# Optimization experiments

Hardware: AMD Instinct MI355X
Metric: run time of the kernel (lower is better)

Reference implementation:

```python
import jax, jax.numpy as jnp
import numpy as np

B, S, HID = 2, 2048, 2048
H, HKV, D = 16, 4, 128
BS = 64            # block_size
TAU = 0.5          # threshold_tau
NB = S // BS       # number of blocks
SCALE = 1.0 / (D ** 0.5)


def _rotate_half(x):
    x1, x2 = x[..., : D // 2], x[..., D // 2 :]
    return jnp.concatenate([-x2, x1], axis=-1)


def setup_inputs() -> dict:
    key = jax.random.key(0)
    k0, k1, k2, k3, k4 = jax.random.split(key, 5)
    hidden_states = jax.random.normal(k0, (B, S, HID), jnp.float32)
    # standard rotary embeddings, [B, S, D] (ndim==3 path of _apply_rotary_pos_emb)
    pos = jnp.arange(S, dtype=jnp.float32)
    inv_freq = 1.0 / (10000.0 ** (jnp.arange(0, D, 2, dtype=jnp.float32) / D))
    emb = jnp.concatenate([pos[:, None] * inv_freq[None, :]] * 2, axis=-1)  # [S, D]
    cos = jnp.broadcast_to(jnp.cos(emb)[None], (B, S, D)).astype(jnp.float32)
    sin = jnp.broadcast_to(jnp.sin(emb)[None], (B, S, D)).astype(jnp.float32)
    Wq = jax.random.normal(k1, (HID, H * D), jnp.float32) * 0.02
    Wk = jax.random.normal(k2, (HID, HKV * D), jnp.float32) * 0.02
    Wv = jax.random.normal(k3, (HID, HKV * D), jnp.float32) * 0.02
    Wo = jax.random.normal(k4, (HID, HID), jnp.float32) * 0.02
    return {"hidden_states": hidden_states, "cos": cos, "sin": sin,
            "Wq": Wq, "Wk": Wk, "Wv": Wv, "Wo": Wo}


def reference(hidden_states, cos, sin, Wq, Wk, Wv, Wo):
    # QKV projections -> [B, heads, S, D]
    q = (hidden_states @ Wq).reshape(B, S, H, D).transpose(0, 2, 1, 3)
    k = (hidden_states @ Wk).reshape(B, S, HKV, D).transpose(0, 2, 1, 3)
    v = (hidden_states @ Wv).reshape(B, S, HKV, D).transpose(0, 2, 1, 3)
    # RoPE (cos/sin [B,S,D] -> broadcast over heads)
    c, s = cos[:, None], sin[:, None]
    q = q * c + _rotate_half(q) * s
    k = k * c + _rotate_half(k) * s
    # GQA repeat_interleave on head dim
    n_rep = H // HKV
    k = jnp.repeat(k, n_rep, axis=1)
    v = jnp.repeat(v, n_rep, axis=1)
    # ---- AttnGate: block-mean pooled Q/K scores -> hard block mask ----
    q_blk = q.reshape(B, H, NB, BS, D).mean(axis=3)  # [B,H,NB,D]
    k_blk = k.reshape(B, H, NB, BS, D).mean(axis=3)
    gate_logits = jnp.einsum('bhid,bhjd->bhij', q_blk, k_blk) * SCALE
    hard = jax.nn.sigmoid(gate_logits) >= TAU                      # [B,H,NB,NB]
    hard = hard | jnp.eye(NB, dtype=bool)                          # keep diagonal blocks
    hard = hard & jnp.tril(jnp.ones((NB, NB), dtype=bool))         # block-causal
    # expand block mask to token level and intersect with causal mask
    tok_mask = jnp.repeat(jnp.repeat(hard, BS, axis=2), BS, axis=3)  # [B,H,S,S]
    tok_mask = tok_mask & jnp.tril(jnp.ones((S, S), dtype=bool))
    # ---- block-sparse (masked) attention ----
    scores = jnp.einsum('bhsd,bhtd->bhst', q, k) * SCALE
    scores = jnp.where(tok_mask, scores, jnp.float32(-1e30))
    probs = jax.nn.softmax(scores.astype(jnp.float32), axis=-1).astype(v.dtype)
    out = jnp.einsum('bhst,bhtd->bhsd', probs, v)
    out = out.transpose(0, 2, 1, 3).reshape(B, S, HID)
    return out @ Wo
```

## Files before the change

kernel.cpp:

```cpp
#include <hip/hip_runtime.h>
#include <stdint.h>

typedef unsigned short u16;
typedef _Float16 half8 __attribute__((ext_vector_type(8)));
typedef float floatx4 __attribute__((ext_vector_type(4)));
typedef u16 u16x4 __attribute__((ext_vector_type(4)));

#define B_ 2
#define S_ 2048
#define HID_ 2048
#define H_ 16
#define HKV_ 4
#define D_ 128
#define NB_ 32
#define SCALE_ 0.08838834764831845f
#define SC_L2 0.12753102331884178f
#define SMAX_L2 5.770780163555852f

__device__ __forceinline__ u16 f2h_bits(float f) {
  _Float16 h = (_Float16)f;
  return __builtin_bit_cast(u16, h);
}

__device__ __forceinline__ void transpose_body(const float* __restrict__ src, u16* __restrict__ dst,
                                               int Kdim, int N, int ldd, int nsplit,
                                               int k0, int n0, float (*tile)[65]) {
#pragma unroll
  for (int p = 0; p < 16; ++p) {
    int e = threadIdx.x + p * 256;
    int r = e >> 6, c = e & 63;
    tile[r][c] = src[(size_t)(k0 + r) * N + n0 + c];
  }
  __syncthreads();
#pragma unroll
  for (int p = 0; p < 16; ++p) {
    int e = threadIdx.x + p * 256;
    int k = e & 63, n = e >> 6;
    float v = tile[k][n];
    for (int s = 0; s < nsplit; ++s) {
      _Float16 hh = (_Float16)v;
      dst[(size_t)(n0 + n) * ldd + s * Kdim + k0 + k] = __builtin_bit_cast(u16, hh);
      v -= (float)hh;
    }
  }
}

__global__ __launch_bounds__(256) void k_prep(const float* __restrict__ hs, u16* __restrict__ A2,
                                              const float* __restrict__ Wq, const float* __restrict__ Wk,
                                              const float* __restrict__ Wv,
                                              u16* __restrict__ B2T, u16* __restrict__ WvT) {
  __shared__ float tile[64][65];
  int id = blockIdx.x;
  if (id < 8192) {
    int idx = id * 256 + threadIdx.x;
    int f0 = idx * 4;
    float4 v = *reinterpret_cast<const float4*>(hs + f0);
    float vv[4] = {v.x, v.y, v.z, v.w};
    u16x4 h0, h1;
#pragma unroll
    for (int e = 0; e < 4; ++e) {
      _Float16 a = (_Float16)vv[e];
      float r = vv[e] - (float)a;
      _Float16 b = (_Float16)r;
      h0[e] = __builtin_bit_cast(u16, a);
      h1[e] = __builtin_bit_cast(u16, b);
    }
    int row = f0 >> 11;
    int col = f0 & 2047;
    *reinterpret_cast<u16x4*>(A2 + (size_t)row * 4096 + col) = h0;
    *reinterpret_cast<u16x4*>(A2 + (size_t)row * 4096 + 2048 + col) = h1;
  } else if (id < 9216) {
    int t = id - 8192;
    transpose_body(Wq, B2T, 2048, 2048, 4096, 2, (t & 31) * 64, (t >> 5) * 64, tile);
  } else if (id < 9472) {
    int t = id - 9216;
    transpose_body(Wk, B2T + (size_t)2048 * 4096, 2048, 512, 4096, 2, (t & 31) * 64, (t >> 5) * 64, tile);
  } else {
    int t = id - 9472;
    transpose_body(Wv, WvT, 2048, 512, 2048, 1, (t & 31) * 64, (t >> 5) * 64, tile);
  }
}

__global__ __launch_bounds__(256) void k_transpose_split(const float* __restrict__ src, u16* __restrict__ dst,
                                                         int Kdim, int N, int ldd, int nsplit) {
  __shared__ float tile[64][65];
  transpose_body(src, dst, Kdim, N, ldd, nsplit, blockIdx.x * 64, blockIdx.y * 64, tile);
}


#define FENCE() __builtin_amdgcn_sched_barrier(0)
#define BAR() do { FENCE(); __builtin_amdgcn_s_barrier(); FENCE(); } while (0)
#define WAITVM(N) do { FENCE(); asm volatile("s_waitcnt vmcnt(" #N ")" ::: "memory"); FENCE(); } while (0)

__device__ __forceinline__ int kmap(int map, int t) {
  return ((map >> ((t >> 5) * 4)) & 15) * 2048 + (t & 31) * 64;
}

__device__ __forceinline__ void stage_half(const u16* __restrict__ src, int sr0, int lda, int kb,
                                           u16* dst, int w, int lane) {
#pragma unroll
  for (int rr = 0; rr < 2; ++rr) {
    int chunk = rr * 8 + w;
    int row = chunk * 8 + (lane >> 3);
    int slot = (lane & 7) ^ (lane >> 3);
    const u16* gp = src + (size_t)(sr0 + row) * lda + kb + slot * 8;
    __builtin_amdgcn_global_load_lds((const __attribute__((address_space(1))) unsigned int*)gp,
                                     (__attribute__((address_space(3))) unsigned int*)(dst + chunk * 512),
                                     16, 0, 0);
  }
}

#define RD_A(mh) do { \
  _Pragma("unroll") \
  for (int m_ = 0; m_ < 4; ++m_) { \
    aF[m_][0] = *reinterpret_cast<const half8*>(&sm[(mh)*8192 + (wm*64 + m_*16 + l15)*64 + ((quad ^ l7) * 8)]); \
    aF[m_][1] = *reinterpret_cast<const half8*>(&sm[(mh)*8192 + (wm*64 + m_*16 + l15)*64 + (((4 + quad) ^ l7) * 8)]); \
  } } while (0)

#define RD_B(nh, BF) do { \
  _Pragma("unroll") \
  for (int n_ = 0; n_ < 2; ++n_) { \
    BF[n_][0] = *reinterpret_cast<const half8*>(&sm[16384 + (nh)*8192 + (wn*32 + n_*16 + l15)*64 + ((quad ^ l7) * 8)]); \
    BF[n_][1] = *reinterpret_cast<const half8*>(&sm[16384 + (nh)*8192 + (wn*32 + n_*16 + l15)*64 + (((4 + quad) ^ l7) * 8)]); \
  } } while (0)

#define MM(mh, nh, BF) do { \
  __builtin_amdgcn_s_setprio(1); \
  _Pragma("unroll") \
  for (int m_ = 0; m_ < 4; ++m_) \
  _Pragma("unroll") \
  for (int n_ = 0; n_ < 2; ++n_) { \
    acc[(mh)*4 + m_][(nh)*2 + n_] = __builtin_amdgcn_mfma_f32_16x16x32_f16(aF[m_][0], BF[n_][0], acc[(mh)*4 + m_][(nh)*2 + n_], 0, 0, 0); \
    acc[(mh)*4 + m_][(nh)*2 + n_] = __builtin_amdgcn_mfma_f32_16x16x32_f16(aF[m_][1], BF[n_][1], acc[(mh)*4 + m_][(nh)*2 + n_], 0, 0, 0); \
  } \
  __builtin_amdgcn_s_setprio(0); } while (0)

__device__ __forceinline__ void gemm256(const u16* __restrict__ A, const u16* __restrict__ BT,
                                        float* __restrict__ C, u16* __restrict__ Ch, u16* sm,
                                        int row0, int col0, int NT,
                                        int lda, int ldb, int ldc, int ldch,
                                        int amap, int bmap) {
  const int tid = (int)threadIdx.x;
  const int lane = tid & 63;
  const int w = tid >> 6;
  const int wm = w >> 2, wn = w & 3;
  const int quad = lane >> 4, l15 = lane & 15, l7 = lane & 7;

  floatx4 acc[8][4];
#pragma unroll
  for (int i = 0; i < 8; ++i)
#pragma unroll
    for (int j = 0; j < 4; ++j) acc[i][j] = (floatx4){0.f, 0.f, 0.f, 0.f};

  half8 aF[4][2], bF0[2][2], bF1[2][2];

  {
    int ka = kmap(amap, 0), kb = kmap(bmap, 0);
    stage_half(A,  row0,       lda, ka, sm + 0,     w, lane);
    stage_half(BT, col0,       ldb, kb, sm + 16384, w, lane);
    stage_half(BT, col0 + 128, ldb, kb, sm + 24576, w, lane);
    stage_half(A,  row0 + 128, lda, ka, sm + 8192,  w, lane);
  }
  WAITVM(4);
  BAR();

  for (int t = 0; t < NT; ++t) {
    int tn = t + 1; if (tn >= NT) tn = 0;
    int kan = kmap(amap, tn), kbn = kmap(bmap, tn);

    RD_A(0); RD_B(0, bF0);
    WAITVM(2);
    BAR(); MM(0, 0, bF0); BAR();
    RD_B(1, bF1);
    stage_half(A,  row0, lda, kan, sm + 0,     w, lane);
    stage_half(BT, col0, ldb, kbn, sm + 16384, w, lane);
    WAITVM(4);
    BAR(); MM(0, 1, bF1); BAR();
    RD_A(1);
    stage_half(BT, col0 + 128, ldb, kbn, sm + 24576, w, lane);
    BAR(); MM(1, 1, bF1); BAR();
    stage_half(A, row0 + 128, lda, kan, sm + 8192, w, lane);
    WAITVM(4);
    BAR(); MM(1, 0, bF0); BAR();
  }
  WAITVM(0);

#pragma unroll
  for (int i = 0; i < 8; ++i) {
    int mh = i >> 2, m = i & 3;
#pragma unroll
    for (int j = 0; j < 4; ++j) {
      int nh = j >> 1, n = j & 1;
#pragma unroll
      for (int r = 0; r < 4; ++r) {
        int rr = row0 + mh * 128 + wm * 64 + m * 16 + quad * 4 + r;
        int cc = col0 + nh * 128 + wn * 32 + n * 16 + l15;
        if (Ch)
          Ch[(size_t)rr * ldch + cc] = f2h_bits(acc[i][j][r]);
        else
          C[(size_t)rr * ldc + cc] = acc[i][j][r];
      }
    }
  }
}


__device__ __forceinline__ void stage_halfA64(const u16* __restrict__ src, int sr0, int lda, int kb,
                                              u16* dst, int w, int lane) {
  int row = w * 8 + (lane >> 3);
  int slot = (lane & 7) ^ (lane >> 3);
  const u16* gp = src + (size_t)(sr0 + row) * lda + kb + slot * 8;
  __builtin_amdgcn_global_load_lds((const __attribute__((address_space(1))) unsigned int*)gp,
                                   (__attribute__((address_space(3))) unsigned int*)(dst + w * 512),
                                   16, 0, 0);
}

#define RD_A128(mh) do { \
  _Pragma("unroll") \
  for (int m_ = 0; m_ < 2; ++m_) { \
    aF[m_][0] = *reinterpret_cast<const half8*>(&sm[(mh)*4096 + (wm*32 + m_*16 + l15)*64 + ((quad ^ l7) * 8)]); \
    aF[m_][1] = *reinterpret_cast<const half8*>(&sm[(mh)*4096 + (wm*32 + m_*16 + l15)*64 + (((4 + quad) ^ l7) * 8)]); \
  } } while (0)

#define RD_B128(nh, BF) do { \
  _Pragma("unroll") \
  for (int n_ = 0; n_ < 2; ++n_) { \
    BF[n_][0] = *reinterpret_cast<const half8*>(&sm[8192 + (nh)*8192 + (wn*32 + n_*16 + l15)*64 + ((quad ^ l7) * 8)]); \
    BF[n_][1] = *reinterpret_cast<const half8*>(&sm[8192 + (nh)*8192 + (wn*32 + n_*16 + l15)*64 + (((4 + quad) ^ l7) * 8)]); \
  } } while (0)

#define MM128(mh, nh, BF) do { \
  __builtin_amdgcn_s_setprio(1); \
  _Pragma("unroll") \
  for (int m_ = 0; m_ < 2; ++m_) \
  _Pragma("unroll") \
  for (int n_ = 0; n_ < 2; ++n_) { \
    acc[(mh)*2 + m_][(nh)*2 + n_] = __builtin_amdgcn_mfma_f32_16x16x32_f16(aF[m_][0], BF[n_][0], acc[(mh)*2 + m_][(nh)*2 + n_], 0, 0, 0); \
    acc[(mh)*2 + m_][(nh)*2 + n_] = __builtin_amdgcn_mfma_f32_16x16x32_f16(aF[m_][1], BF[n_][1], acc[(mh)*2 + m_][(nh)*2 + n_], 0, 0, 0); \
  } \
  __builtin_amdgcn_s_setprio(0); } while (0)

__device__ __forceinline__ void gemm128(const u16* __restrict__ A, const u16* __restrict__ BT,
                                        float* __restrict__ C, u16* sm,
                                        int row0, int col0, int NT,
                                        int lda, int ldb, int ldc) {
  const int tid = (int)threadIdx.x;
  const int lane = tid & 63;
  const int w = tid >> 6;
  const int wm = w >> 2, wn = w & 3;
  const int quad = lane >> 4, l15 = lane & 15, l7 = lane & 7;

  floatx4 acc[4][4];
#pragma unroll
  for (int i = 0; i < 4; ++i)
#pragma unroll
    for (int j = 0; j < 4; ++j) acc[i][j] = (floatx4){0.f, 0.f, 0.f, 0.f};

  half8 aF[2][2], bF0[2][2], bF1[2][2];

  stage_halfA64(A,  row0,      lda, 0, sm + 0,     w, lane);
  stage_half  (BT, col0,       ldb, 0, sm + 8192,  w, lane);
  stage_half  (BT, col0 + 128, ldb, 0, sm + 16384, w, lane);
  stage_halfA64(A,  row0 + 64, lda, 0, sm + 4096,  w, lane);
  WAITVM(3);
  BAR();

  for (int t = 0; t < NT; ++t) {
    int tn = t + 1; if (tn >= NT) tn = 0;
    int kn = tn * 64;

    RD_A128(0); RD_B128(0, bF0);
    WAITVM(1);
    BAR(); MM128(0, 0, bF0); BAR();
    RD_B128(1, bF1);
    stage_halfA64(A,  row0, lda, kn, sm + 0,    w, lane);
    stage_half  (BT, col0, ldb, kn, sm + 8192,  w, lane);
    WAITVM(3);
    BAR(); MM128(0, 1, bF1); BAR();
    RD_A128(1);
    stage_half(BT, col0 + 128, ldb, kn, sm + 16384, w, lane);
    BAR(); MM128(1, 1, bF1); BAR();
    stage_halfA64(A, row0 + 64, lda, kn, sm + 4096, w, lane);
    WAITVM(3);
    BAR(); MM128(1, 0, bF0); BAR();
  }
  WAITVM(0);

#pragma unroll
  for (int i = 0; i < 4; ++i) {
    int mh = i >> 1, m = i & 1;
#pragma unroll
    for (int j = 0; j < 4; ++j) {
      int nh = j >> 1, n = j & 1;
#pragma unroll
      for (int r = 0; r < 4; ++r) {
        int rr = row0 + mh * 64 + wm * 32 + m * 16 + quad * 4 + r;
        int cc = col0 + nh * 128 + wn * 32 + n * 16 + l15;
        C[(size_t)rr * ldc + cc] = acc[i][j][r];
      }
    }
  }
}

__global__ __launch_bounds__(512) void k_gemm_qkv(const u16* __restrict__ A2, const u16* __restrict__ B2T,
                                                  const u16* __restrict__ WvT, float* __restrict__ qkv,
                                                  u16* __restrict__ corr) {
  __shared__ u16 sm[32768];
  int id = blockIdx.x;
  if (id < 160) {
    int lg = (id & 7) * 20 + (id >> 3);
    int row0 = (lg / 10) * 256, col0 = (lg % 10) * 256;
    gemm256(A2, B2T, nullptr, corr, sm, row0, col0, 64, 4096, 4096, 0, 2560, 0x01, 0x10);
  } else if (id < 320) {
    int t = id - 160;
    int lg = (t & 7) * 20 + (t >> 3);
    int row0 = (lg / 10) * 256, col0 = (lg % 10) * 256;
    gemm256(A2, B2T, qkv, nullptr, sm, row0, col0, 32, 4096, 4096, 3072, 0, 0, 0);
  } else {
    int t = id - 320;
    int row0 = (t >> 1) * 256, col0 = (t & 1) * 256;
    gemm256(A2, WvT, qkv + 2560, nullptr, sm, row0, col0, 32, 4096, 2048, 3072, 0, 0, 0);
  }
}

__global__ __launch_bounds__(512) void k_gemm_wo(const u16* __restrict__ attn, const u16* __restrict__ WoT,
                                                 float* __restrict__ out) {
  __shared__ u16 sm[24576];
  int id = blockIdx.x;
  gemm128(attn, WoT, out, sm, (id >> 3) * 128, (id & 7) * 256, 32, 2048, 2048, 2048);
}

__global__ __launch_bounds__(256) void k_rope_mean(const float* __restrict__ qkv, const u16* __restrict__ corr,
                                                   const float* __restrict__ cosb, const float* __restrict__ sinb,
                                                   u16* __restrict__ qbf, u16* __restrict__ kbf,
                                                   float* __restrict__ qblk, float* __restrict__ kblk) {
  int cc = blockIdx.x, i = blockIdx.y, b = blockIdx.z;
  int c = cc * 256 + threadIdx.x;
  bool isq = c < 2048;
  int hh = isq ? (c >> 7) : ((c - 2048) >> 7);
  int d = isq ? (c & 127) : ((c - 2048) & 127);
  int pairc = (d < 64) ? c + 64 : c - 64;
  float sgn = (d < 64) ? -1.0f : 1.0f;
  int row0 = b * S_ + i * 64;
  float sum = 0.0f;
  for (int s = 0; s < 64; ++s) {
    int row = row0 + s;
    float x1 = qkv[(size_t)row * 3072 + c]
             + (float)__builtin_bit_cast(_Float16, corr[(size_t)row * 2560 + c]);
    float x2 = qkv[(size_t)row * 3072 + pairc]
             + (float)__builtin_bit_cast(_Float16, corr[(size_t)row * 2560 + pairc]);
    float cv = cosb[(size_t)row * 128 + d];
    float sv = sinb[(size_t)row * 128 + d];
    float val = x1 * cv + sgn * x2 * sv;
    sum += val;
    if (isq)
      qbf[((size_t)(b * H_ + hh) * S_ + i * 64 + s) * 128 + d] = f2h_bits(val);
    else
      kbf[((size_t)(b * HKV_ + hh) * S_ + i * 64 + s) * 128 + d] = f2h_bits(val);
  }
  if (isq)
    qblk[((size_t)(b * H_ + hh) * NB_ + i) * 128 + d] = sum * 0.015625f;
  else
    kblk[((size_t)(b * HKV_ + hh) * NB_ + i) * 128 + d] = sum * 0.015625f;
}

__global__ __launch_bounds__(256) void k_vlayout(const float* __restrict__ qkv, u16* __restrict__ vT) {
  int i = blockIdx.x, hk = blockIdx.y, b = blockIdx.z;
  __shared__ u16 tile[64 * 130];
#pragma unroll
  for (int p = 0; p < 32; ++p) {
    int e = threadIdx.x + p * 256;
    int s = e >> 7, d = e & 127;
    float v = qkv[(size_t)(b * S_ + i * 64 + s) * 3072 + 2560 + hk * 128 + d];
    tile[s * 130 + d] = f2h_bits(v);
  }
  __syncthreads();
#pragma unroll
  for (int p = 0; p < 32; ++p) {
    int e = threadIdx.x + p * 256;
    int d2 = e >> 6, s2 = e & 63;
    vT[((size_t)(b * HKV_ + hk) * 128 + d2) * S_ + i * 64 + s2] = tile[s2 * 130 + d2];
  }
}

__global__ __launch_bounds__(256) void k_gate(const float* __restrict__ qblk, const float* __restrict__ kblk,
                                              int* __restrict__ mask) {
  int h = blockIdx.x, b = blockIdx.y;
  int hk = h >> 2;
  __shared__ float qs[32 * 128];
  __shared__ float ks[32 * 128];
  size_t qb0 = (size_t)(b * H_ + h) * NB_ * 128;
  size_t kb0 = (size_t)(b * HKV_ + hk) * NB_ * 128;
#pragma unroll
  for (int p = 0; p < 16; ++p) {
    int e = threadIdx.x + p * 256;
    qs[e] = qblk[qb0 + e];
    ks[e] = kblk[kb0 + e];
  }
  __syncthreads();
#pragma unroll
  for (int p = 0; p < 4; ++p) {
    int l = threadIdx.x + p * 256;
    int i = l >> 5, j = l & 31;
    int m;
    if (j > i) m = 0;
    else if (j == i) m = 1;
    else {
      float dot = 0.0f;
      for (int d = 0; d < 128; ++d) dot += qs[i * 128 + d] * ks[j * 128 + d];
      m = (dot >= 0.0f) ? 1 : 0;
    }
    mask[((size_t)(b * H_ + h) * NB_ + i) * NB_ + j] = m;
  }
}

__global__ __launch_bounds__(256) void k_flash(const u16* __restrict__ qbf, const u16* __restrict__ kbf,
                                               const u16* __restrict__ vT, const int* __restrict__ mask,
                                               u16* __restrict__ attn) {
  const int id = blockIdx.x;
  const int i = 31 - (id >> 5);
  const int hb = id & 31;
  const int h = hb & 15, b = hb >> 4;
  const int hk = h >> 2;
  const int tid = threadIdx.x;
  const int lane = tid & 63;
  const int w = tid >> 6;
  const int quad = lane >> 4;
  const int l15 = lane & 15;

  __shared__ u16 Ksb[2 * 64 * 128];
  __shared__ u16 Vsb[2 * 128 * 64];
  __shared__ u16 Ps[4 * 16 * 64];

  half8 qF[4];
  const u16* qbase = qbf + ((size_t)(b * H_ + h) * S_ + i * 64 + w * 16 + l15) * 128;
#pragma unroll
  for (int kk = 0; kk < 4; ++kk)
    qF[kk] = *reinterpret_cast<const half8*>(qbase + kk * 32 + quad * 8);

  floatx4 o[8];
#pragma unroll
  for (int t = 0; t < 8; ++t) o[t] = (floatx4){0.f, 0.f, 0.f, 0.f};
  float ls[4] = {0.f, 0.f, 0.f, 0.f};

  const u16* kb = kbf + (size_t)(b * HKV_ + hk) * S_ * 128;
  const u16* vb = vT + (size_t)(b * HKV_ + hk) * 128 * S_;
  const int* mrp = mask + ((size_t)(b * H_ + h) * NB_ + i) * NB_;

#define FSTAGE(J, BUF) do { \
  _Pragma("unroll") \
  for (int t_ = 0; t_ < 4; ++t_) { \
    int g2 = t_ * 4 + w; \
    int stok = g2 * 4 + (lane >> 4); \
    int ul = (lane & 15) ^ (stok & 15); \
    const u16* srcK = kb + (size_t)((J) * 64 + stok) * 128 + ul * 8; \
    __builtin_amdgcn_global_load_lds((const __attribute__((address_space(1))) unsigned int*)srcK, \
                                     (__attribute__((address_space(3))) unsigned int*)(Ksb + (BUF) * 8192 + g2 * 512), \
                                     16, 0, 0); \
    int sdd = g2 * 8 + (lane >> 3); \
    int ulv = (lane & 7) ^ (sdd & 7); \
    const u16* srcV = vb + (size_t)sdd * S_ + (J) * 64 + ulv * 8; \
    __builtin_amdgcn_global_load_lds((const __attribute__((address_space(1))) unsigned int*)srcV, \
                                     (__attribute__((address_space(3))) unsigned int*)(Vsb + (BUF) * 8192 + g2 * 512), \
                                     16, 0, 0); \
  } } while (0)

  int jcur = 0;
  while (!mrp[jcur]) ++jcur;
  FSTAGE(jcur, 0);
  int cur = 0;

  for (;;) {
    int jn = jcur + 1;
    while (jn <= i && !mrp[jn]) ++jn;
    bool hn = (jn <= i);
    if (hn) { FSTAGE(jn, cur ^ 1); WAITVM(8); }
    else    { WAITVM(0); }
    BAR();

    const u16* Kc = Ksb + cur * 8192;
    const u16* Vc = Vsb + cur * 8192;
#pragma unroll
    for (int ct = 0; ct < 4; ++ct) {
      floatx4 cacc = (floatx4){0.f, 0.f, 0.f, 0.f};
#pragma unroll
      for (int kk = 0; kk < 4; ++kk) {
        int phys = (kk * 4 + quad) ^ l15;
        half8 bF = *reinterpret_cast<const half8*>(&Kc[(ct * 16 + l15) * 128 + phys * 8]);
        cacc = __builtin_amdgcn_mfma_f32_16x16x32_f16(qF[kk], bF, cacc, 0, 0, 0);
      }
#pragma unroll
      for (int r = 0; r < 4; ++r) {
        float s = cacc[r];
        if (jcur == i && (ct * 16 + l15) > (w * 16 + quad * 4 + r)) s = -1e30f;
        float p = __builtin_exp2f(fmaf(s, SC_L2, -SMAX_L2));
        _Float16 ph = (_Float16)p;
        ls[r] += (float)ph;
        Ps[w * 1024 + (quad * 4 + r) * 64 + ct * 16 + l15] = __builtin_bit_cast(u16, ph);
      }
    }
#pragma unroll
    for (int kk2 = 0; kk2 < 2; ++kk2) {
      half8 aP = *reinterpret_cast<const half8*>(&Ps[w * 1024 + l15 * 64 + kk2 * 32 + quad * 8]);
#pragma unroll
      for (int ct2 = 0; ct2 < 8; ++ct2) {
        int phys = (kk2 * 4 + quad) ^ (l15 & 7);
        half8 bV = *reinterpret_cast<const half8*>(&Vc[(ct2 * 16 + l15) * 64 + phys * 8]);
        o[ct2] = __builtin_amdgcn_mfma_f32_16x16x32_f16(aP, bV, o[ct2], 0, 0, 0);
      }
    }
    BAR();
    if (!hn) break;
    jcur = jn; cur ^= 1;
  }

#pragma unroll
  for (int xm = 1; xm < 16; xm <<= 1)
#pragma unroll
    for (int r = 0; r < 4; ++r) ls[r] += __shfl_xor(ls[r], xm, 64);
  float invl[4];
#pragma unroll
  for (int r = 0; r < 4; ++r) invl[r] = 1.0f / ls[r];
#pragma unroll
  for (int ct2 = 0; ct2 < 8; ++ct2)
#pragma unroll
    for (int r = 0; r < 4; ++r) {
      size_t row = (size_t)(b * S_ + i * 64 + w * 16 + quad * 4 + r);
      attn[row * 2048 + h * 128 + ct2 * 16 + l15] = f2h_bits(o[ct2][r] * invl[r]);
    }
}

extern "C" void kernel_launch(void* const* d_in, const int* in_sizes, int n_in,
                              void* d_out, int out_size, void* d_ws, size_t ws_size,
                              hipStream_t stream) {
  const float* hs = (const float*)d_in[0];
  const float* cosb = (const float*)d_in[1];
  const float* sinb = (const float*)d_in[2];
  const float* Wq = (const float*)d_in[3];
  const float* Wk = (const float*)d_in[4];
  const float* Wv = (const float*)d_in[5];
  const float* Wo = (const float*)d_in[6];
  float* out = (float*)d_out;
  char* ws = (char*)d_ws;

  u16* A2 = (u16*)(ws + 0);
  u16* B2T = (u16*)(ws + 33554432);
  u16* WvT = (u16*)(ws + 54525952);
  float* qkv = (float*)(ws + 56623104);
  u16* corr = (u16*)out;
  u16* attn = (u16*)(ws + 0);
  u16* qbf = (u16*)(ws + 16777216);
  u16* kbf = (u16*)(ws + 33554432);
  u16* vTbf = (u16*)(ws + 37748736);
  float* qblk = (float*)(ws + 41943040);
  float* kblk = (float*)(ws + 42467328);
  int* mask = (int*)(ws + 42598400);
  u16* WoT = (u16*)(ws + 43122688);

  (void)in_sizes; (void)n_in; (void)out_size; (void)ws_size;

  k_prep<<<9728, 256, 0, stream>>>(hs, A2, Wq, Wk, Wv, B2T, WvT);

  k_gemm_qkv<<<352, 512, 0, stream>>>(A2, B2T, WvT, qkv, corr);

  k_transpose_split<<<dim3(32, 32), 256, 0, stream>>>(Wo, WoT, 2048, 2048, 2048, 1);

  k_rope_mean<<<dim3(10, 32, 2), 256, 0, stream>>>(qkv, corr, cosb, sinb, qbf, kbf, qblk, kblk);
  k_vlayout<<<dim3(32, 4, 2), 256, 0, stream>>>(qkv, vTbf);

  k_gate<<<dim3(16, 2), 256, 0, stream>>>(qblk, kblk, mask);

  k_flash<<<1024, 256, 0, stream>>>(qbf, kbf, vTbf, mask, attn);

  k_gemm_wo<<<256, 512, 0, stream>>>(attn, WoT, out);
}
```

Measured before the change: 388.5 us.

## Drop pre-MFMA barriers in GEMM loops and merge mid-stage kernels into one launch

Removes the barrier that preceded each MFMA block in both the 256- and 128-tile GEMM main loops, keeping only the barrier after each compute step. This is meant to cut synchronisation stalls between waves. It also fuses the RoPE/block-mean, Wo transpose and V-layout kernels into a single block-indexed launch, removing two launches and letting the independent work run concurrently. The risk is an LDS race if the removed barriers were protecting visibility of asynchronously staged tiles.

New measurement: 369.6 us. 1.05x faster.

```diff
diff --git a/kernel.cpp b/kernel.cpp
--- a/kernel.cpp
+++ b/kernel.cpp
@@ -81,12 +81,6 @@
   }
 }
 
-__global__ __launch_bounds__(256) void k_transpose_split(const float* __restrict__ src, u16* __restrict__ dst,
-                                                         int Kdim, int N, int ldd, int nsplit) {
-  __shared__ float tile[64][65];
-  transpose_body(src, dst, Kdim, N, ldd, nsplit, blockIdx.x * 64, blockIdx.y * 64, tile);
-}
-
 
 #define FENCE() __builtin_amdgcn_sched_barrier(0)
 #define BAR() do { FENCE(); __builtin_amdgcn_s_barrier(); FENCE(); } while (0)
@@ -170,18 +164,18 @@
 
     RD_A(0); RD_B(0, bF0);
     WAITVM(2);
-    BAR(); MM(0, 0, bF0); BAR();
+    MM(0, 0, bF0); BAR();
     RD_B(1, bF1);
     stage_half(A,  row0, lda, kan, sm + 0,     w, lane);
     stage_half(BT, col0, ldb, kbn, sm + 16384, w, lane);
     WAITVM(4);
-    BAR(); MM(0, 1, bF1); BAR();
+    MM(0, 1, bF1); BAR();
     RD_A(1);
     stage_half(BT, col0 + 128, ldb, kbn, sm + 24576, w, lane);
-    BAR(); MM(1, 1, bF1); BAR();
+    MM(1, 1, bF1); BAR();
     stage_half(A, row0 + 128, lda, kan, sm + 8192, w, lane);
     WAITVM(4);
-    BAR(); MM(1, 0, bF0); BAR();
+    MM(1, 0, bF0); BAR();
   }
   WAITVM(0);
 
@@ -271,18 +265,18 @@
 
     RD_A128(0); RD_B128(0, bF0);
     WAITVM(1);
-    BAR(); MM128(0, 0, bF0); BAR();
+    MM128(0, 0, bF0); BAR();
     RD_B128(1, bF1);
     stage_halfA64(A,  row0, lda, kn, sm + 0,    w, lane);
     stage_half  (BT, col0, ldb, kn, sm + 8192,  w, lane);
     WAITVM(3);
-    BAR(); MM128(0, 1, bF1); BAR();
+    MM128(0, 1, bF1); BAR();
     RD_A128(1);
     stage_half(BT, col0 + 128, ldb, kn, sm + 16384, w, lane);
-    BAR(); MM128(1, 1, bF1); BAR();
+    MM128(1, 1, bF1); BAR();
     stage_halfA64(A, row0 + 64, lda, kn, sm + 4096, w, lane);
     WAITVM(3);
-    BAR(); MM128(1, 0, bF0); BAR();
+    MM128(1, 0, bF0); BAR();
   }
   WAITVM(0);
 
@@ -330,56 +324,66 @@
   gemm128(attn, WoT, out, sm, (id >> 3) * 128, (id & 7) * 256, 32, 2048, 2048, 2048);
 }
 
-__global__ __launch_bounds__(256) void k_rope_mean(const float* __restrict__ qkv, const u16* __restrict__ corr,
-                                                   const float* __restrict__ cosb, const float* __restrict__ sinb,
-                                                   u16* __restrict__ qbf, u16* __restrict__ kbf,
-                                                   float* __restrict__ qblk, float* __restrict__ kblk) {
-  int cc = blockIdx.x, i = blockIdx.y, b = blockIdx.z;
-  int c = cc * 256 + threadIdx.x;
-  bool isq = c < 2048;
-  int hh = isq ? (c >> 7) : ((c - 2048) >> 7);
-  int d = isq ? (c & 127) : ((c - 2048) & 127);
-  int pairc = (d < 64) ? c + 64 : c - 64;
-  float sgn = (d < 64) ? -1.0f : 1.0f;
-  int row0 = b * S_ + i * 64;
-  float sum = 0.0f;
-  for (int s = 0; s < 64; ++s) {
-    int row = row0 + s;
-    float x1 = qkv[(size_t)row * 3072 + c]
-             + (float)__builtin_bit_cast(_Float16, corr[(size_t)row * 2560 + c]);
-    float x2 = qkv[(size_t)row * 3072 + pairc]
-             + (float)__builtin_bit_cast(_Float16, corr[(size_t)row * 2560 + pairc]);
-    float cv = cosb[(size_t)row * 128 + d];
-    float sv = sinb[(size_t)row * 128 + d];
-    float val = x1 * cv + sgn * x2 * sv;
-    sum += val;
+__global__ __launch_bounds__(256) void k_mid(const float* __restrict__ qkv, const u16* __restrict__ corr,
+                                             const float* __restrict__ cosb, const float* __restrict__ sinb,
+                                             u16* __restrict__ qbf, u16* __restrict__ kbf,
+                                             float* __restrict__ qblk, float* __restrict__ kblk,
+                                             const float* __restrict__ Wo, u16* __restrict__ WoT,
+                                             u16* __restrict__ vT) {
+  __shared__ __align__(16) char smem[16640];
+  int id = blockIdx.x;
+  if (id < 640) {
+    int t = id;
+    int cc = t % 10, i = (t / 10) & 31, b = t / 320;
+    int c = cc * 256 + (int)threadIdx.x;
+    bool isq = c < 2048;
+    int hh = isq ? (c >> 7) : ((c - 2048) >> 7);
+    int d = isq ? (c & 127) : ((c - 2048) & 127);
+    int pairc = (d < 64) ? c + 64 : c - 64;
+    float sgn = (d < 64) ? -1.0f : 1.0f;
+    int row0 = b * S_ + i * 64;
+    float sum = 0.0f;
+    for (int s = 0; s < 64; ++s) {
+      int row = row0 + s;
+      float x1 = qkv[(size_t)row * 3072 + c]
+               + (float)__builtin_bit_cast(_Float16, corr[(size_t)row * 2560 + c]);
+      float x2 = qkv[(size_t)row * 3072 + pairc]
+               + (float)__builtin_bit_cast(_Float16, corr[(size_t)row * 2560 + pairc]);
+      float cv = cosb[(size_t)row * 128 + d];
+      float sv = sinb[(size_t)row * 128 + d];
+      float val = x1 * cv + sgn * x2 * sv;
+      sum += val;
+      if (isq)
+        qbf[((size_t)(b * H_ + hh) * S_ + i * 64 + s) * 128 + d] = f2h_bits(val);
+      else
+        kbf[((size_t)(b * HKV_ + hh) * S_ + i * 64 + s) * 128 + d] = f2h_bits(val);
+    }
     if (isq)
-      qbf[((size_t)(b * H_ + hh) * S_ + i * 64 + s) * 128 + d] = f2h_bits(val);
+      qblk[((size_t)(b * H_ + hh) * NB_ + i) * 128 + d] = sum * 0.015625f;
     else
-      kbf[((size_t)(b * HKV_ + hh) * S_ + i * 64 + s) * 128 + d] = f2h_bits(val);
-  }
-  if (isq)
-    qblk[((size_t)(b * H_ + hh) * NB_ + i) * 128 + d] = sum * 0.015625f;
-  else
-    kblk[((size_t)(b * HKV_ + hh) * NB_ + i) * 128 + d] = sum * 0.015625f;
-}
-
-__global__ __launch_bounds__(256) void k_vlayout(const float* __restrict__ qkv, u16* __restrict__ vT) {
-  int i = blockIdx.x, hk = blockIdx.y, b = blockIdx.z;
-  __shared__ u16 tile[64 * 130];
-#pragma unroll
-  for (int p = 0; p < 32; ++p) {
-    int e = threadIdx.x + p * 256;
-    int s = e >> 7, d = e & 127;
-    float v = qkv[(size_t)(b * S_ + i * 64 + s) * 3072 + 2560 + hk * 128 + d];
-    tile[s * 130 + d] = f2h_bits(v);
-  }
-  __syncthreads();
-#pragma unroll
-  for (int p = 0; p < 32; ++p) {
-    int e = threadIdx.x + p * 256;
-    int d2 = e >> 6, s2 = e & 63;
-    vT[((size_t)(b * HKV_ + hk) * 128 + d2) * S_ + i * 64 + s2] = tile[s2 * 130 + d2];
+      kblk[((size_t)(b * HKV_ + hh) * NB_ + i) * 128 + d] = sum * 0.015625f;
+  } else if (id < 1664) {
+    int t = id - 640;
+    transpose_body(Wo, WoT, 2048, 2048, 2048, 1, (t & 31) * 64, (t >> 5) * 64,
+                   reinterpret_cast<float(*)[65]>(smem));
+  } else {
+    int t = id - 1664;
+    int i = t & 31, hk = (t >> 5) & 3, b = t >> 7;
+    u16* tile = (u16*)smem;
+#pragma unroll
+    for (int p = 0; p < 32; ++p) {
+      int e = threadIdx.x + p * 256;
+      int s = e >> 7, d = e & 127;
+      float v = qkv[(size_t)(b * S_ + i * 64 + s) * 3072 + 2560 + hk * 128 + d];
+      tile[s * 130 + d] = f2h_bits(v);
+    }
+    __syncthreads();
+#pragma unroll
+    for (int p = 0; p < 32; ++p) {
+      int e = threadIdx.x + p * 256;
+      int d2 = e >> 6, s2 = e & 63;
+      vT[((size_t)(b * HKV_ + hk) * 128 + d2) * S_ + i * 64 + s2] = tile[s2 * 130 + d2];
+    }
   }
 }
 
@@ -563,10 +567,7 @@
 
   k_gemm_qkv<<<352, 512, 0, stream>>>(A2, B2T, WvT, qkv, corr);
 
-  k_transpose_split<<<dim3(32, 32), 256, 0, stream>>>(Wo, WoT, 2048, 2048, 2048, 1);
-
-  k_rope_mean<<<dim3(10, 32, 2), 256, 0, stream>>>(qkv, corr, cosb, sinb, qbf, kbf, qblk, kblk);
-  k_vlayout<<<dim3(32, 4, 2), 256, 0, stream>>>(qkv, vTbf);
+  k_mid<<<1920, 256, 0, stream>>>(qkv, corr, cosb, sinb, qbf, kbf, qblk, kblk, Wo, WoT, vTbf);
 
   k_gate<<<dim3(16, 2), 256, 0, stream>>>(qblk, kblk, mask);
 
```
